# Kernel optimization log

Hardware: AMD Instinct MI355X
Metric: run time of the kernel (lower is better)

Reference implementation:

```python
import jax, jax.numpy as jnp
import numpy as np

TOP_K = 2
ROUTED_SCALING = 1.0


def setup_inputs() -> dict:
    key = jax.random.key(0)
    k1, k2, k3, k4 = jax.random.split(key, 4)
    S, B, H = 1024, 2, 1024
    E, FFN = 8, 1408
    return {
        "hidden_states": jax.random.normal(k1, (S, B, H), dtype=jnp.float32),
        "gate_w": jax.random.normal(k2, (E, H), dtype=jnp.float32) * 0.02,
        "w1": jax.random.normal(k3, (E, H, 2 * FFN), dtype=jnp.float32) * 0.02,
        "w2": jax.random.normal(k4, (E, FFN, H), dtype=jnp.float32) * 0.02,
    }


def reference(hidden_states, gate_w, w1, w2):
    # hidden_states: [S, B, H] -> transpose(0,1) as in MoELayer.forward
    x = jnp.transpose(hidden_states, (1, 0, 2))  # [B, S, H]
    B, S, H = x.shape
    E = gate_w.shape[0]
    xt = x.reshape(-1, H)  # [T, H], T = B*S
    T = xt.shape[0]

    # --- TopKGate ('greedy', softmax scoring) ---
    scores = jax.nn.softmax(xt @ gate_w.T, axis=-1)  # [T, E]
    topk_w, topk_idx = jax.lax.top_k(scores, TOP_K)  # [T, K]
    # norm_topk_prob: normalize the top-k weights
    topk_w = topk_w / (jnp.sum(topk_w, axis=-1, keepdims=True) + 1e-20)
    topk_w = topk_w * ROUTED_SCALING

    # Sparse combine weights [T, E] (zero for non-selected experts)
    combine = jnp.zeros((T, E), dtype=xt.dtype)
    combine = combine.at[jnp.arange(T)[:, None], topk_idx].set(topk_w)

    # --- Experts: per-expert swiglu MLP, weighted combine ---
    # Equivalent math to dispatch -> per-expert grouped GEMM -> combine:
    # non-selected experts contribute with weight 0.
    out = jnp.zeros_like(xt)
    for e in range(E):
        h = xt @ w1[e]                      # [T, 2*FFN]
        g, u = jnp.split(h, 2, axis=-1)
        y = (jax.nn.silu(g) * u) @ w2[e]    # [T, H]
        out = out + combine[:, e:e + 1] * y

    out = out.reshape(B, S, H)
    return jnp.transpose(out, (1, 0, 2))  # back to [S, B, H]
```

## Files before the change

### kernel.cpp

```cpp
#include <hip/hip_runtime.h>
#include <hip/hip_bf16.h>

#define S_      1024
#define B_      2
#define H_      1024
#define E_      8
#define FFN_    1408
#define TWO_FFN 2816
#define T_      2048
#define MAXSLOTS 5120
#define NB_CONV 512
#define TSZ     (128 * 64)

typedef float  f32x4 __attribute__((ext_vector_type(4)));
typedef short  s16x8 __attribute__((ext_vector_type(8)));

__device__ __forceinline__ unsigned short f2bf(float f) {
    unsigned u = __float_as_uint(f);
    u += 0x7fffu + ((u >> 16) & 1u);
    return (unsigned short)(u >> 16);
}
__device__ __forceinline__ unsigned pk2(float a, float b) {
    __hip_bfloat162 h = __float22bfloat162_rn(make_float2(a, b));
    unsigned u; __builtin_memcpy(&u, &h, 4); return u;
}
__device__ __forceinline__ void async16(const void* g, void* l) {
    __builtin_amdgcn_global_load_lds(
        (const __attribute__((address_space(1))) unsigned int*)(unsigned long long)g,
        (__attribute__((address_space(3))) unsigned int*)(unsigned long long)l,
        16, 0, 0);
}
__device__ __forceinline__ size_t xrow_off(int t) {
    return (size_t)(t & (S_ - 1)) * (B_ * H_) + (size_t)(t >> 10) * H_;
}

__device__ __forceinline__ void load8(f32x4 v[8], const float* __restrict__ p, size_t C) {
#pragma unroll
    for (int j = 0; j < 8; j++) v[j] = *(const f32x4*)(p + (size_t)j * C);
}
__device__ __forceinline__ void stage_wr(const f32x4 v[8], unsigned* __restrict__ base,
                                         const int off[4]) {
#pragma unroll
    for (int i = 0; i < 4; i++) {
        uint4 q;
        q.x = pk2(v[0][i], v[1][i]);
        q.y = pk2(v[2][i], v[3][i]);
        q.z = pk2(v[4][i], v[5][i]);
        q.w = pk2(v[6][i], v[7][i]);
        *(uint4*)(base + off[i]) = q;
    }
}
__device__ __forceinline__ void mfma_step(const unsigned short* __restrict__ As,
                                          const unsigned short* __restrict__ Bs,
                                          f32x4 acc[4][4], int rowB, int colB, int lane) {
    int sw = (lane & 7) << 3;
#pragma unroll
    for (int kk = 0; kk < 64; kk += 32) {
        int kr = (kk + ((lane >> 4) << 3)) ^ sw;
        s16x8 af[4], bf[4];
#pragma unroll
        for (int mi = 0; mi < 4; mi++) af[mi] = *(const s16x8*)&As[(rowB + mi * 16 + (lane & 15)) * 64 + kr];
#pragma unroll
        for (int ni = 0; ni < 4; ni++) bf[ni] = *(const s16x8*)&Bs[(colB + ni * 16 + (lane & 15)) * 64 + kr];
#pragma unroll
        for (int mi = 0; mi < 4; mi++)
#pragma unroll
            for (int ni = 0; ni < 4; ni++)
                acc[mi][ni] = __builtin_amdgcn_mfma_f32_16x16x32_bf16(af[mi], bf[ni], acc[mi][ni], 0, 0, 0);
    }
}

__global__ void k_prep(const float* __restrict__ hs, const float* __restrict__ gw,
                       unsigned short* __restrict__ xb,
                       int* __restrict__ topkI, float* __restrict__ topkW) {
    int cb = blockIdx.x, tid = threadIdx.x;
    int wid = tid >> 6, lane = tid & 63;
    int t = cb * 4 + wid;
    const float* xr = hs + xrow_off(t);
    unsigned short* xo = xb + (size_t)t * H_;
    float acc[E_];
#pragma unroll
    for (int e = 0; e < E_; e++) acc[e] = 0.f;
#pragma unroll
    for (int p = 0; p < 4; p++) {
        int h = p * 256 + lane * 4;
        const float4 v = *(const float4*)(xr + h);
        unsigned short o[4] = { f2bf(v.x), f2bf(v.y), f2bf(v.z), f2bf(v.w) };
        *(uint2*)(xo + h) = *(const uint2*)o;
#pragma unroll
        for (int e = 0; e < E_; e++) {
            const float4 g = *(const float4*)(gw + e * H_ + h);
            acc[e] += v.x * g.x + v.y * g.y + v.z * g.z + v.w * g.w;
        }
    }
#pragma unroll
    for (int e = 0; e < E_; e++)
        for (int off = 32; off > 0; off >>= 1) acc[e] += __shfl_down(acc[e], off);
    if (lane == 0) {
        float l0 = -1e30f, l1 = -1e30f; int i0 = 0, i1 = 0;
#pragma unroll
        for (int e = 0; e < E_; e++) {
            float v = acc[e];
            if (v > l0)      { l1 = l0; i1 = i0; l0 = v; i0 = e; }
            else if (v > l1) { l1 = v;  i1 = e; }
        }
        float p1 = expf(l1 - l0);
        float w0 = 1.f / (1.f + p1);
        float w1s = 1.f - w0;
        topkI[2 * t] = i0; topkI[2 * t + 1] = i1;
        topkW[2 * t] = w0; topkW[2 * t + 1] = w1s;
    }
}

__global__ void k_routeassign(const int* __restrict__ topkI, const float* __restrict__ topkW,
                              int* __restrict__ ctrl, int* __restrict__ perm,
                              int* __restrict__ slotOfTok) {
    __shared__ int s_wcnt[4][E_];
    __shared__ int s_base[E_];
    __shared__ int s_cur[E_];
    int tid = threadIdx.x, wid = tid >> 6, lane = tid & 63;
    int cnt[E_];
#pragma unroll
    for (int j = 0; j < E_; j++) cnt[j] = 0;
    for (int i = tid; i < 2 * T_; i += 256) {
        int e = topkI[i];
#pragma unroll
        for (int j = 0; j < E_; j++) cnt[j] += (e == j);
    }
#pragma unroll
    for (int j = 0; j < E_; j++)
        for (int off = 32; off > 0; off >>= 1) cnt[j] += __shfl_down(cnt[j], off);
    if (lane == 0) {
#pragma unroll
        for (int j = 0; j < E_; j++) s_wcnt[wid][j] = cnt[j];
    }
    __syncthreads();
    if (tid == 0) {
        int b = 0;
        for (int e = 0; e < E_; e++) {
            int n = s_wcnt[0][e] + s_wcnt[1][e] + s_wcnt[2][e] + s_wcnt[3][e];
            int ntile = (n + 127) >> 7;
            s_base[e] = b;
            ctrl[40 + e] = ntile;
            ctrl[48 + e] = b;
            b += ntile * 128;
        }
#pragma unroll
        for (int e = 0; e < E_; e++) s_cur[e] = 0;
    }
    __syncthreads();
    for (int s = tid; s < MAXSLOTS; s += 256) perm[s] = 0;
    __syncthreads();
    for (int t = tid; t < T_; t += 256) {
#pragma unroll
        for (int k = 0; k < 2; k++) {
            int e = topkI[2 * t + k];
            int pos = atomicAdd(&s_cur[e], 1);
            int slot = s_base[e] + pos;
            perm[slot] = t;
            slotOfTok[2 * t + k] = slot;
        }
    }
}

__global__ __launch_bounds__(256, 2) void k_gemm1(
    const unsigned short* __restrict__ xb, const float* __restrict__ w1,
    const int* __restrict__ ctrl, const int* __restrict__ perm,
    unsigned short* __restrict__ A2) {
    int b  = blockIdx.x;
    int p  = ((b >> 7) << 3) | (b & 7);
    int ti = (b >> 3) & 15;
    int e  = p / 22;
    int ct = p - e * 22;
    if (ti >= ctrl[40 + e]) return;
    int slot0 = ctrl[48 + e] + ti * 128;
    __shared__ __align__(16) unsigned short smem[2 * TSZ];
    unsigned short* As = smem;
    unsigned short* Bs = smem + TSZ;
    int tid = threadIdx.x, wid = tid >> 6, lane = tid & 63;

    const unsigned short* aPtr[4];
    int lAoff[4];
#pragma unroll
    for (int i = 0; i < 4; i++) {
        int c = (wid * 4 + i) * 64 + lane;
        int r = c >> 3;
        int qd = (c & 7) ^ (r & 7);
        int tok = perm[slot0 + r];
        aPtr[i] = xb + (size_t)tok * H_ + qd * 8;
        lAoff[i] = c * 8;
    }
    int h1 = tid >> 7, kp = (tid >> 4) & 7, nq = tid & 15;
    int rb = h1 * 64 + nq * 4;
    const float* bsrc = w1 + (size_t)e * (H_ * TWO_FFN)
                        + (h1 ? (FFN_ + ct * 64) : (ct * 64)) + nq * 4
                        + (size_t)(kp * 8) * TWO_FFN;
    int bwOff[4];
#pragma unroll
    for (int i = 0; i < 4; i++)
        bwOff[i] = (rb + i) * 32 + ((kp ^ ((rb + i) & 7)) << 2);

    f32x4 acc[4][4];
#pragma unroll
    for (int mi = 0; mi < 4; mi++)
#pragma unroll
        for (int ni = 0; ni < 4; ni++) acc[mi][ni] = (f32x4){0.f, 0.f, 0.f, 0.f};
    int wm = wid & 1, wn = wid >> 1;
    int rowB = wm * 64, colB = wn * 64;

    f32x4 bv[8];
    load8(bv, bsrc, TWO_FFN);
    stage_wr(bv, (unsigned*)Bs, bwOff);
#pragma unroll
    for (int i = 0; i < 4; i++) async16(aPtr[i], As + lAoff[i]);
    load8(bv, bsrc + (size_t)64 * TWO_FFN, TWO_FFN);
    __syncthreads();

#pragma unroll 1
    for (int s = 0; s < 16; s++) {
        mfma_step(As, Bs, acc, rowB, colB, lane);
        if (s == 15) break;
        __syncthreads();
        stage_wr(bv, (unsigned*)Bs, bwOff);
        size_t ka = (size_t)(s + 1) * 64;
#pragma unroll
        for (int i = 0; i < 4; i++) async16(aPtr[i] + ka, As + lAoff[i]);
        if (s < 14) load8(bv, bsrc + (size_t)(s + 2) * 64 * TWO_FFN, TWO_FFN);
        __syncthreads();
    }
    __syncthreads();
    float* upLds = (float*)smem;
    if (wn == 1) {
#pragma unroll
        for (int mi = 0; mi < 4; mi++)
#pragma unroll
            for (int ni = 0; ni < 4; ni++)
#pragma unroll
                for (int r = 0; r < 4; r++) {
                    int m = rowB + mi * 16 + (lane >> 4) * 4 + r;
                    int u = ni * 16 + (lane & 15);
                    upLds[m * 64 + u] = acc[mi][ni][r];
                }
    }
    __syncthreads();
    if (wn == 0) {
#pragma unroll
        for (int mi = 0; mi < 4; mi++)
#pragma unroll
            for (int r = 0; r < 4; r++) {
                int m = rowB + mi * 16 + (lane >> 4) * 4 + r;
                unsigned short* arow = A2 + (size_t)(slot0 + m) * FFN_ + ct * 64;
#pragma unroll
                for (int ni = 0; ni < 4; ni++) {
                    int gl = ni * 16 + (lane & 15);
                    float g = acc[mi][ni][r];
                    float u = upLds[m * 64 + gl];
                    float s = g / (1.f + expf(-g));
                    arow[gl] = f2bf(s * u);
                }
            }
    }
}

__global__ __launch_bounds__(256, 2) void k_gemm2(
    const unsigned short* __restrict__ A2, const float* __restrict__ w2,
    const int* __restrict__ ctrl, unsigned short* __restrict__ Yp) {
    int b  = blockIdx.x;
    int p  = ((b >> 7) << 3) | (b & 7);
    int ti = (b >> 3) & 15;
    int e  = p >> 4;
    int ct = (p >> 1) & 7;
    int ks = p & 1;
    if (ti >= ctrl[40 + e]) return;
    int slot0 = ctrl[48 + e] + ti * 128;
    __shared__ __align__(16) unsigned short As[TSZ];
    __shared__ __align__(16) unsigned short Bs[TSZ];
    int tid = threadIdx.x, wid = tid >> 6, lane = tid & 63;

    const unsigned short* aPtr[4];
    int lAoff[4];
#pragma unroll
    for (int i = 0; i < 4; i++) {
        int c = (wid * 4 + i) * 64 + lane;
        int r = c >> 3;
        int qd = (c & 7) ^ (r & 7);
        aPtr[i] = A2 + (size_t)(slot0 + r) * FFN_ + qd * 8;
        lAoff[i] = c * 8;
    }
    int h1 = tid >> 7, kp = (tid >> 4) & 7, nq = tid & 15;
    int rb = h1 * 64 + nq * 4;
    int kbeg = ks * (FFN_ / 2);
    const float* bsrc = w2 + (size_t)e * (FFN_ * H_)
                        + ct * 128 + h1 * 64 + nq * 4
                        + (size_t)(kp * 8 + kbeg) * H_;
    int bwOff[4];
#pragma unroll
    for (int i = 0; i < 4; i++)
        bwOff[i] = (rb + i) * 32 + ((kp ^ ((rb + i) & 7)) << 2);

    f32x4 acc[4][4];
#pragma unroll
    for (int mi = 0; mi < 4; mi++)
#pragma unroll
        for (int ni = 0; ni < 4; ni++) acc[mi][ni] = (f32x4){0.f, 0.f, 0.f, 0.f};
    int wm = wid & 1, wn = wid >> 1;
    int rowB = wm * 64, colB = wn * 64;

    f32x4 bv[8];
    load8(bv, bsrc, H_);
    stage_wr(bv, (unsigned*)Bs, bwOff);
#pragma unroll
    for (int i = 0; i < 4; i++) async16(aPtr[i] + kbeg, As + lAoff[i]);
    load8(bv, bsrc + (size_t)64 * H_, H_);
    __syncthreads();

#pragma unroll 1
    for (int s = 0; s < 11; s++) {
        mfma_step(As, Bs, acc, rowB, colB, lane);
        if (s == 10) break;
        __syncthreads();
        stage_wr(bv, (unsigned*)Bs, bwOff);
        size_t ka = (size_t)(s + 1) * 64;
#pragma unroll
        for (int i = 0; i < 4; i++) async16(aPtr[i] + kbeg + ka, As + lAoff[i]);
        if (s < 9) load8(bv, bsrc + (size_t)(s + 2) * 64 * H_, H_);
        __syncthreads();
    }
    unsigned short* yp = Yp + (size_t)ks * MAXSLOTS * H_;
#pragma unroll
    for (int mi = 0; mi < 4; mi++)
#pragma unroll
        for (int r = 0; r < 4; r++) {
            int m = rowB + mi * 16 + (lane >> 4) * 4 + r;
#pragma unroll
            for (int ni = 0; ni < 4; ni++) {
                int n = colB + ni * 16 + (lane & 15);
                yp[(size_t)(slot0 + m) * H_ + ct * 128 + n] = f2bf(acc[mi][ni][r]);
            }
        }
}

__global__ void k_combine(const unsigned short* __restrict__ Yp, const int* __restrict__ slotOfTok,
                          const float* __restrict__ topkW, float* __restrict__ out) {
    int t = blockIdx.x;
    int h = threadIdx.x * 4;
    int sA = slotOfTok[2 * t], sB = slotOfTok[2 * t + 1];
    float wA = topkW[2 * t],   wB = topkW[2 * t + 1];
    const unsigned short* pA0 = Yp + (size_t)sA * H_ + h;
    const unsigned short* pA1 = Yp + ((size_t)MAXSLOTS + sA) * H_ + h;
    const unsigned short* pB0 = Yp + (size_t)sB * H_ + h;
    const unsigned short* pB1 = Yp + ((size_t)MAXSLOTS + sB) * H_ + h;
    unsigned short a0[4], a1[4], b0[4], b1[4];
    *(uint2*)a0 = *(const uint2*)pA0;
    *(uint2*)a1 = *(const uint2*)pA1;
    *(uint2*)b0 = *(const uint2*)pB0;
    *(uint2*)b1 = *(const uint2*)pB1;
    float4 r;
    float* rp = (float*)&r;
#pragma unroll
    for (int i = 0; i < 4; i++) {
        float av = __uint_as_float(((unsigned)a0[i]) << 16) + __uint_as_float(((unsigned)a1[i]) << 16);
        float bv = __uint_as_float(((unsigned)b0[i]) << 16) + __uint_as_float(((unsigned)b1[i]) << 16);
        rp[i] = wA * av + wB * bv;
    }
    *(float4*)(out + xrow_off(t) + h) = r;
}

extern "C" void kernel_launch(void* const* d_in, const int* in_sizes, int n_in,
                              void* d_out, int out_size, void* d_ws, size_t ws_size,
                              hipStream_t stream) {
    (void)in_sizes; (void)n_in; (void)ws_size; (void)out_size;
    const float* hs = (const float*)d_in[0];
    const float* gw = (const float*)d_in[1];
    const float* w1 = (const float*)d_in[2];
    const float* w2 = (const float*)d_in[3];
    float* out = (float*)d_out;
    char* ws = (char*)d_ws;

    int*            ctrl   = (int*)ws;
    int*            topkI  = (int*)(ws + (16u << 10));
    float*          topkW  = (float*)(ws + (48u << 10));
    int*            perm   = (int*)(ws + (80u << 10));
    int*            slotOfTok = (int*)(ws + (144u << 10));
    unsigned short* xb    = (unsigned short*)(ws + (1ull  << 20));
    unsigned short* A2    = (unsigned short*)(ws + (8ull  << 20));
    unsigned short* Yp    = (unsigned short*)(ws + (24ull << 20));

    k_prep<<<NB_CONV, 256, 0, stream>>>(hs, gw, xb, topkI, topkW);
    k_routeassign<<<1, 256, 0, stream>>>(topkI, topkW, ctrl, perm, slotOfTok);
    k_gemm1<<<dim3(22 * 128), 256, 0, stream>>>(xb, w1, ctrl, perm, A2);
    k_gemm2<<<dim3(16 * 128), 256, 0, stream>>>(A2, w2, ctrl, Yp);
    k_combine<<<2048, 256, 0, stream>>>(Yp, slotOfTok, topkW, out);
}
```

Baseline: 268.2 us.

## Use compact tile list for grouped GEMM grids and issue A loads earlier

The routing kernel now builds a flat list of active 128-row tiles (slot base and expert per tile) plus a tile count. Both GEMM kernels index into this list, so the grid shrinks from 128 tiles per column to at most 40 and far fewer blocks launch only to exit. Block order also changes: consecutive blocks now walk tiles within the same column tile, which shifts which weight columns are loaded together and changes L2 reuse. Separately, the async A-tile loads are issued before the B staging writes to start that global-to-LDS traffic sooner.

After: 280.6 us. +4.6%, slower.

```diff
diff --git a/kernel.cpp b/kernel.cpp
--- a/kernel.cpp
+++ b/kernel.cpp
@@ -9,6 +9,7 @@
 #define TWO_FFN 2816
 #define T_      2048
 #define MAXSLOTS 5120
+#define MAXTILES 40
 #define NB_CONV 512
 #define TSZ     (128 * 64)
 
@@ -136,15 +137,21 @@
     }
     __syncthreads();
     if (tid == 0) {
-        int b = 0;
+        int b = 0, nt = 0;
         for (int e = 0; e < E_; e++) {
             int n = s_wcnt[0][e] + s_wcnt[1][e] + s_wcnt[2][e] + s_wcnt[3][e];
             int ntile = (n + 127) >> 7;
             s_base[e] = b;
             ctrl[40 + e] = ntile;
             ctrl[48 + e] = b;
+            for (int i = 0; i < ntile; i++) {
+                ctrl[64 + nt]  = b + i * 128;
+                ctrl[104 + nt] = e;
+                nt++;
+            }
             b += ntile * 128;
         }
+        ctrl[39] = nt;
 #pragma unroll
         for (int e = 0; e < E_; e++) s_cur[e] = 0;
     }
@@ -168,12 +175,11 @@
     const int* __restrict__ ctrl, const int* __restrict__ perm,
     unsigned short* __restrict__ A2) {
     int b  = blockIdx.x;
-    int p  = ((b >> 7) << 3) | (b & 7);
-    int ti = (b >> 3) & 15;
-    int e  = p / 22;
-    int ct = p - e * 22;
-    if (ti >= ctrl[40 + e]) return;
-    int slot0 = ctrl[48 + e] + ti * 128;
+    int tt = b % MAXTILES;
+    int ct = b / MAXTILES;
+    if (tt >= ctrl[39]) return;
+    int e     = ctrl[104 + tt];
+    int slot0 = ctrl[64 + tt];
     __shared__ __align__(16) unsigned short smem[2 * TSZ];
     unsigned short* As = smem;
     unsigned short* Bs = smem + TSZ;
@@ -221,10 +227,10 @@
         mfma_step(As, Bs, acc, rowB, colB, lane);
         if (s == 15) break;
         __syncthreads();
+        size_t ka = (size_t)(s + 1) * 64;
+#pragma unroll
+        for (int i = 0; i < 4; i++) async16(aPtr[i] + ka, As + lAoff[i]);
         stage_wr(bv, (unsigned*)Bs, bwOff);
-        size_t ka = (size_t)(s + 1) * 64;
-#pragma unroll
-        for (int i = 0; i < 4; i++) async16(aPtr[i] + ka, As + lAoff[i]);
         if (s < 14) load8(bv, bsrc + (size_t)(s + 2) * 64 * TWO_FFN, TWO_FFN);
         __syncthreads();
     }
@@ -266,13 +272,13 @@
     const unsigned short* __restrict__ A2, const float* __restrict__ w2,
     const int* __restrict__ ctrl, unsigned short* __restrict__ Yp) {
     int b  = blockIdx.x;
-    int p  = ((b >> 7) << 3) | (b & 7);
-    int ti = (b >> 3) & 15;
-    int e  = p >> 4;
-    int ct = (p >> 1) & 7;
-    int ks = p & 1;
-    if (ti >= ctrl[40 + e]) return;
-    int slot0 = ctrl[48 + e] + ti * 128;
+    int tt = b % MAXTILES;
+    int q  = b / MAXTILES;
+    int ct = q >> 1;
+    int ks = q & 1;
+    if (tt >= ctrl[39]) return;
+    int e     = ctrl[104 + tt];
+    int slot0 = ctrl[64 + tt];
     __shared__ __align__(16) unsigned short As[TSZ];
     __shared__ __align__(16) unsigned short Bs[TSZ];
     int tid = threadIdx.x, wid = tid >> 6, lane = tid & 63;
@@ -319,10 +325,10 @@
         mfma_step(As, Bs, acc, rowB, colB, lane);
         if (s == 10) break;
         __syncthreads();
+        size_t ka = (size_t)(s + 1) * 64;
+#pragma unroll
+        for (int i = 0; i < 4; i++) async16(aPtr[i] + kbeg + ka, As + lAoff[i]);
         stage_wr(bv, (unsigned*)Bs, bwOff);
-        size_t ka = (size_t)(s + 1) * 64;
-#pragma unroll
-        for (int i = 0; i < 4; i++) async16(aPtr[i] + kbeg + ka, As + lAoff[i]);
         if (s < 9) load8(bv, bsrc + (size_t)(s + 2) * 64 * H_, H_);
         __syncthreads();
     }
@@ -388,7 +394,7 @@
 
     k_prep<<<NB_CONV, 256, 0, stream>>>(hs, gw, xb, topkI, topkW);
     k_routeassign<<<1, 256, 0, stream>>>(topkI, topkW, ctrl, perm, slotOfTok);
-    k_gemm1<<<dim3(22 * 128), 256, 0, stream>>>(xb, w1, ctrl, perm, A2);
-    k_gemm2<<<dim3(16 * 128), 256, 0, stream>>>(A2, w2, ctrl, Yp);
+    k_gemm1<<<dim3(22 * MAXTILES), 256, 0, stream>>>(xb, w1, ctrl, perm, A2);
+    k_gemm2<<<dim3(16 * MAXTILES), 256, 0, stream>>>(A2, w2, ctrl, Yp);
     k_combine<<<2048, 256, 0, stream>>>(Yp, slotOfTok, topkW, out);
 }
```
